# Optimization experiments

Hardware: AMD Instinct MI355X
Metric: run time of the kernel (lower is better)

The kernel has to match this reference:

```python
import jax, jax.numpy as jnp
import numpy as np

N_NODES = 50000
N_EDGES = 800000
F_IN = 128
HID = 128
F_ADD = 32
N_GRAPHS = 128


def setup_inputs() -> dict:
    key = jax.random.key(0)
    ks = jax.random.split(key, 12)
    x = jax.random.normal(ks[0], (N_NODES, F_IN), dtype=jnp.float32)
    edge_index = jax.random.randint(ks[1], (2, N_EDGES), 0, N_NODES, dtype=jnp.int64)
    batch = jnp.sort(jax.random.randint(ks[2], (N_NODES,), 0, N_GRAPHS, dtype=jnp.int64))
    additional_features = jax.random.normal(ks[3], (N_GRAPHS, F_ADD), dtype=jnp.float32)
    def glorot(k, shape):
        fan_in, fan_out = shape[0], shape[1]
        lim = jnp.sqrt(6.0 / (fan_in + fan_out)).astype(jnp.float32)
        return jax.random.uniform(k, shape, jnp.float32, -lim, lim)
    W1 = glorot(ks[4], (F_IN, HID)); b1 = jnp.zeros((HID,), jnp.float32)
    W2 = glorot(ks[5], (HID, HID)); b2 = jnp.zeros((HID,), jnp.float32)
    fc1_w = glorot(ks[6], (HID + F_ADD, HID)); fc1_b = jnp.zeros((HID,), jnp.float32)
    fc2_w = glorot(ks[7], (HID, 2)); fc2_b = jnp.zeros((2,), jnp.float32)
    return {"x": x, "edge_index": edge_index, "batch": batch,
            "additional_features": additional_features,
            "W1": W1, "b1": b1, "W2": W2, "b2": b2,
            "fc1_w": fc1_w, "fc1_b": fc1_b, "fc2_w": fc2_w, "fc2_b": fc2_b}


def _gcn_conv(h, src, dst, norm, W, b):
    # h: [N, d_in]; symmetric-normalized scatter-add aggregation (PyG GCNConv)
    h = h @ W                                   # [N, d_out]
    msg = h[src] * norm[:, None]                # gather + scale: [E+N, d_out]
    return jax.ops.segment_sum(msg, dst, num_segments=N_NODES) + b


def reference(x, edge_index, batch, additional_features,
              W1, b1, W2, b2, fc1_w, fc1_b, fc2_w, fc2_b):
    loops = jnp.arange(N_NODES, dtype=edge_index.dtype)
    src = jnp.concatenate([edge_index[0], loops])   # A + I
    dst = jnp.concatenate([edge_index[1], loops])
    deg = jax.ops.segment_sum(jnp.ones_like(src, dtype=x.dtype), dst,
                              num_segments=N_NODES)
    dinv = jnp.where(deg > 0, jax.lax.rsqrt(jnp.maximum(deg, 1.0)), 0.0)
    norm = dinv[src] * dinv[dst]

    h = jax.nn.relu(_gcn_conv(x, src, dst, norm, W1, b1))
    h = jax.nn.relu(_gcn_conv(h, src, dst, norm, W2, b2))
    # dropout is identity in eval mode

    sums = jax.ops.segment_sum(h, batch, num_segments=N_GRAPHS)    # [G, HID]
    counts = jax.ops.segment_sum(jnp.ones((N_NODES,), h.dtype), batch,
                                 num_segments=N_GRAPHS)
    pooled = sums / jnp.maximum(counts, 1.0)[:, None]              # global_mean_pool

    z = jnp.concatenate([pooled, additional_features], axis=1)     # [G, HID+F_ADD]
    z = jax.nn.relu(z @ fc1_w + fc1_b)
    return z @ fc2_w + fc2_b                                       # [G, 2]
```

## Files before the change

### kernel.cpp

```cpp
#include <hip/hip_runtime.h>

#define NN 50000
#define NE 800000
#define FD 128
#define FDH 64
#define FA 32
#define NG 128
#define EETOT (NE + NN)
#define NBLK ((NN + 255) / 256)
#define FEPB 2048
#define FNCH ((EETOT + FEPB - 1) / FEPB)
#define NPXCD 6250

typedef __attribute__((ext_vector_type(8))) short short8;
typedef __attribute__((ext_vector_type(4))) float f32x4;

__device__ __forceinline__ float bfbits(unsigned short u) {
    return __uint_as_float(((unsigned int)u) << 16);
}
__device__ __forceinline__ float bflo(unsigned int p) { return __uint_as_float(p << 16); }
__device__ __forceinline__ float bfhi(unsigned int p) { return __uint_as_float(p & 0xffff0000u); }
__device__ __forceinline__ unsigned short f2bf(float f) {
    unsigned int u = __float_as_uint(f);
    unsigned int r = u + 0x7FFFu + ((u >> 16) & 1u);
    return (unsigned short)(r >> 16);
}
__device__ __forceinline__ unsigned int packbf(float a, float b) {
    return (unsigned int)f2bf(a) | ((unsigned int)f2bf(b) << 16);
}

__device__ __forceinline__ int wave_probe_bf16(const unsigned int* t, int nwords) {
    int lane = threadIdx.x & 63;
    unsigned int wv = (lane < nwords) ? t[lane] : 0u;
    int nzp = (wv != 0u) ? 1 : 0;
    unsigned int e = (wv >> 7) & 0xFFu;
    int hitp = (nzp && e >= 100u && e <= 140u) ? 1 : 0;
    int nz = __popcll(__ballot(nzp));
    int hits = __popcll(__ballot(hitp));
    return (nz < 8) ? 1 : (hits * 4 >= nz * 3);
}
__device__ __forceinline__ int wave_probe_is64(const int* ei) {
    int lane = threadIdx.x & 63;
    int v = (lane < 32) ? ei[2 * lane + 1] : 0;
    return (__ballot(v != 0) == 0ull) ? 1 : 0;
}

__global__ __launch_bounds__(128) void mark_kernel(float* out, float v) {
    out[threadIdx.x] = v;
}

__global__ __launch_bounds__(256) void prep(
        const void* addf, const void* w1, const void* b1, const void* w2,
        const void* b2, const void* fc1w, const void* fc1b, const void* fc2w,
        const void* fc2b, unsigned int* W1t, unsigned int* W2t,
        float* addff, float* b1f, float* b2f, float* fc1wf, float* fc1bf,
        float* fc2wf, float* fc2bf, int* degi, int* tsum) {
    int b = blockIdx.x;
    if (b < 64) {
        int rel = b * 256 + threadIdx.x;
        const void* src = (rel < 8192) ? w1 : w2;
        unsigned int* dst = (rel < 8192) ? W1t : W2t;
        int flag = wave_probe_bf16((const unsigned int*)src, 64);
        int rr = rel & 8191;
        int n = rr >> 6, kk = rr & 63;
        float lo, hi;
        if (flag) {
            const unsigned short* s = (const unsigned short*)src;
            lo = bfbits(s[(2 * kk) * FD + n]);
            hi = bfbits(s[(2 * kk + 1) * FD + n]);
        } else {
            const float* s = (const float*)src;
            lo = s[(2 * kk) * FD + n];
            hi = s[(2 * kk + 1) * FD + n];
        }
        dst[rr] = packbf(lo, hi);
    } else if (b < 163) {
        int i = (b - 64) * 256 + threadIdx.x;
        int wb = (b - 64) * 256 + (threadIdx.x & ~63);
        const void* src; float* dst; int base; int prnw; int lim;
        if      (wb < 4096)  { src = addf; dst = addff; base = 0;     prnw = 64; lim = 4096;  }
        else if (wb < 4224)  { src = b1;   dst = b1f;   base = 4096;  prnw = 64; lim = 128;   }
        else if (wb < 4352)  { src = b2;   dst = b2f;   base = 4224;  prnw = 64; lim = 128;   }
        else if (wb < 24832) { src = fc1w; dst = fc1wf; base = 4352;  prnw = 64; lim = 20480; }
        else if (wb < 24960) { src = fc1b; dst = fc1bf; base = 24832; prnw = 64; lim = 128;   }
        else if (wb < 25216) { src = fc2w; dst = fc2wf; base = 24960; prnw = 64; lim = 256;   }
        else if (wb < 25280) { src = fc2b; dst = fc2bf; base = 25216; prnw = 1;  lim = 2;     }
        else return;
        int flag = wave_probe_bf16((const unsigned int*)src, prnw);
        int rel = i - base;
        if (rel < lim) {
            if (flag) dst[rel] = bfbits(((const unsigned short*)src)[rel]);
            else      dst[rel] = ((const float*)src)[rel];
        }
    } else {
        int i = (b - 163) * 256 + threadIdx.x;
        if      (i < NN)       degi[i] = 0;
        else if (i < NN + 256) tsum[i - NN] = 0;
    }
}

__global__ __launch_bounds__(256) void deg_kernel(const int* ei, int* deg,
                                                  int* s32, int* d32) {
    int is64 = wave_probe_is64(ei);
    int e = blockIdx.x * 256 + threadIdx.x;
    if (e < NE) {
        int s = is64 ? ei[2 * e] : ei[e];
        int d = is64 ? ei[2 * (NE + e)] : ei[NE + e];
        s32[e] = s;
        d32[e] = d;
        atomicAdd(&deg[d], 1);
    }
}

__global__ __launch_bounds__(256) void scan_fused(const int* degi, const int* batch,
        int* tsum, float* dinv, int* rowstart, int* cursor, int* gstart) {
    __shared__ int sh[256];
    int b = blockIdx.x, t = threadIdx.x;
    int i = b * 256 + t;
    int d = (i < NN) ? degi[i] : 0;
    if (i < NN) dinv[i] = rsqrtf((float)(d + 1));
    int v = (i < NN) ? d + 1 : 0;
    sh[t] = v;
    __syncthreads();
    for (int off = 1; off < 256; off <<= 1) {
        int a = (t >= off) ? sh[t - off] : 0;
        __syncthreads();
        sh[t] += a;
        __syncthreads();
    }
    int incl = sh[t];
    int total = sh[255];
    if (t == 0) atomicExch(&tsum[b], total);
    int pt = 0;
    for (int j = t; j < b; j += 256) {
        int s;
        do { s = atomicAdd(&tsum[j], 0); } while (s == 0);
        pt += s;
    }
    __syncthreads();
    sh[t] = pt;
    __syncthreads();
    for (int off = 128; off >= 1; off >>= 1) {
        if (t < off) sh[t] += sh[t + off];
        __syncthreads();
    }
    int boff = sh[0];
    if (i < NN) {
        int r = boff + incl - v;
        rowstart[i] = r;
        cursor[i]   = r;
    }
    if (i == 0) rowstart[NN] = EETOT;
    if (i < NN) {
        int is64 = (batch[NN - 1] == 0) ? 1 : 0;
        int bc = is64 ? batch[2 * i] : batch[i];
        if (i == 0) {
            for (int g = 0; g <= bc; ++g) gstart[g] = 0;
        } else {
            int bp = is64 ? batch[2 * (i - 1)] : batch[i - 1];
            for (int g = bp + 1; g <= bc; ++g) gstart[g] = i;
        }
        if (i == NN - 1) {
            for (int g = bc + 1; g <= NG; ++g) gstart[g] = NN;
        }
    }
}

__global__ __launch_bounds__(256) void fill_kernel(const int* s32, const int* d32,
        const float* dinv, int* cursor, unsigned int* cv) {
    int chunk = blockIdx.x >> 3;
    int par   = blockIdx.x & 7;
    int base  = chunk * FEPB;
    #pragma unroll
    for (int k = 0; k < FEPB / 256; ++k) {
        int e = base + k * 256 + threadIdx.x;
        if (e >= EETOT) break;
        int s, d;
        if (e < NE) { d = d32[e]; s = -1; }
        else        { s = d = e - NE; }
        if (d / NPXCD != par) continue;
        if (s < 0) s = s32[e];
        int pos = atomicAdd(&cursor[d], 1);
        cv[pos] = (unsigned int)s | ((unsigned int)f2bf(dinv[s] * dinv[d]) << 16);
    }
}

__global__ __launch_bounds__(256) void gemm_mfma(const void* __restrict__ Av,
        const unsigned int* __restrict__ Wt, unsigned short* __restrict__ C,
        int maybe_f32) {
    int wave = threadIdx.x >> 6;
    int lane = threadIdx.x & 63;
    int quad = lane >> 4;
    int l16  = lane & 15;
    int mbase = blockIdx.x * 64 + wave * 16;
    int ra = mbase + l16;
    if (ra >= NN) ra = NN - 1;
    bool f32in = false;
    if (maybe_f32) f32in = !wave_probe_bf16((const unsigned int*)Av, 64);
    short8 af[4];
    if (!f32in) {
        const uint4* Arow = (const uint4*)((const unsigned int*)Av + (size_t)ra * FDH);
        #pragma unroll
        for (int kk = 0; kk < 4; ++kk) {
            uint4 v = Arow[kk * 4 + quad];
            af[kk] = *(short8*)&v;
        }
    } else {
        const float* Arow = (const float*)Av + (size_t)ra * FD;
        #pragma unroll
        for (int kk = 0; kk < 4; ++kk) {
            const float4* p = (const float4*)(Arow + (kk * 4 + quad) * 8);
            float4 u = p[0], v = p[1];
            uint4 q;
            q.x = packbf(u.x, u.y); q.y = packbf(u.z, u.w);
            q.z = packbf(v.x, v.y); q.w = packbf(v.z, v.w);
            af[kk] = *(short8*)&q;
        }
    }
    #pragma unroll
    for (int nt = 0; nt < 8; ++nt) {
        int n = nt * 16 + l16;
        const uint4* Wrow = (const uint4*)(Wt + (size_t)n * FDH);
        f32x4 acc = {0.f, 0.f, 0.f, 0.f};
        #pragma unroll
        for (int kk = 0; kk < 4; ++kk) {
            uint4 wv = Wrow[kk * 4 + quad];
            short8 bf = *(short8*)&wv;
            acc = __builtin_amdgcn_mfma_f32_16x16x32_bf16(af[kk], bf, acc, 0, 0, 0);
        }
        int row0 = mbase + quad * 4;
        #pragma unroll
        for (int reg = 0; reg < 4; ++reg) {
            int r = row0 + reg;
            if (r < NN) C[(size_t)r * FD + nt * 16 + l16] = f2bf(acc[reg]);
        }
    }
}

__global__ __launch_bounds__(256) void aggregate_kernel(const unsigned int* Hb,
        const unsigned int* cv, const int* rowstart, const float* bias,
        unsigned int* outb) {
    int lane = threadIdx.x & 63;
    int half = lane >> 5;
    int c2   = lane & 31;
    int wv   = threadIdx.x >> 6;
    int n = blockIdx.x * 8 + wv * 2 + half;
    const uint2* H2 = (const uint2*)Hb;
    int jb = rowstart[n], je = rowstart[n + 1];
    float a0 = 0.f, a1 = 0.f, a2 = 0.f, a3 = 0.f;
    int j = jb;
    for (; j + 7 < je; j += 8) {
        unsigned int rr[8]; uint2 hh[8];
        #pragma unroll
        for (int k = 0; k < 8; ++k) rr[k] = cv[j + k];
        #pragma unroll
        for (int k = 0; k < 8; ++k) hh[k] = H2[(size_t)(rr[k] & 0xFFFFu) * 32 + c2];
        #pragma unroll
        for (int k = 0; k < 8; ++k) {
            float v = bfbits((unsigned short)(rr[k] >> 16));
            a0 += v * bflo(hh[k].x); a1 += v * bfhi(hh[k].x);
            a2 += v * bflo(hh[k].y); a3 += v * bfhi(hh[k].y);
        }
    }
    for (; j + 3 < je; j += 4) {
        unsigned int rr[4]; uint2 hh[4];
        #pragma unroll
        for (int k = 0; k < 4; ++k) rr[k] = cv[j + k];
        #pragma unroll
        for (int k = 0; k < 4; ++k) hh[k] = H2[(size_t)(rr[k] & 0xFFFFu) * 32 + c2];
        #pragma unroll
        for (int k = 0; k < 4; ++k) {
            float v = bfbits((unsigned short)(rr[k] >> 16));
            a0 += v * bflo(hh[k].x); a1 += v * bfhi(hh[k].x);
            a2 += v * bflo(hh[k].y); a3 += v * bfhi(hh[k].y);
        }
    }
    for (; j < je; ++j) {
        unsigned int r = cv[j];
        uint2 h = H2[(size_t)(r & 0xFFFFu) * 32 + c2];
        float v = bfbits((unsigned short)(r >> 16));
        a0 += v * bflo(h.x); a1 += v * bfhi(h.x);
        a2 += v * bflo(h.y); a3 += v * bfhi(h.y);
    }
    a0 = fmaxf(a0 + bias[4 * c2],     0.f);
    a1 = fmaxf(a1 + bias[4 * c2 + 1], 0.f);
    a2 = fmaxf(a2 + bias[4 * c2 + 2], 0.f);
    a3 = fmaxf(a3 + bias[4 * c2 + 3], 0.f);
    uint2 out;
    out.x = packbf(a0, a1);
    out.y = packbf(a2, a3);
    ((uint2*)outb)[(size_t)n * 32 + c2] = out;
}

__global__ __launch_bounds__(256) void poolhead(const unsigned int* Hb,
        const int* gstart, const float* addf, const float* fc1w, const float* fc1b,
        const float* fc2w, const float* fc2b, const unsigned int* x, void* outp) {
    int g = blockIdx.x;
    int t = threadIdx.x;
    int q = t >> 6, w = t & 63;
    int obf = wave_probe_bf16(x, 64);
    int s = gstart[g], e = gstart[g + 1];
    float a0 = 0.f, a1 = 0.f;
    #pragma unroll 4
    for (int n = s + q; n < e; n += 4) {
        unsigned int h = Hb[(size_t)n * FDH + w];
        a0 += bflo(h);
        a1 += bfhi(h);
    }
    __shared__ float pp[4][FD];
    __shared__ float z[FD + FA];
    __shared__ float h[FD];
    pp[q][2 * w]     = a0;
    pp[q][2 * w + 1] = a1;
    __syncthreads();
    if (t < FD) {
        float cnt = (float)(e - s);
        if (cnt < 1.0f) cnt = 1.0f;
        z[t] = (pp[0][t] + pp[1][t] + pp[2][t] + pp[3][t]) / cnt;
    }
    if (t >= FD && t < FD + FA) z[t] = addf[g * FA + (t - FD)];
    __syncthreads();
    if (t < FD) {
        float acc = fc1b[t];
        #pragma unroll 4
        for (int k = 0; k < FD + FA; ++k)
            acc += z[k] * fc1w[k * FD + t];
        h[t] = fmaxf(acc, 0.f);
    }
    __syncthreads();
    if (t < 2) {
        float o = fc2b[t];
        for (int j = 0; j < FD; ++j) o += h[j] * fc2w[j * 2 + t];
        if (obf) ((unsigned short*)outp)[g * 2 + t] = f2bf(o);
        else     ((float*)outp)[g * 2 + t] = o;
    }
}

extern "C" void kernel_launch(void* const* d_in, const int* in_sizes, int n_in,
                              void* d_out, int out_size, void* d_ws, size_t ws_size,
                              hipStream_t stream) {
    (void)out_size;

    if (n_in != 12) {
        hipLaunchKernelGGL(mark_kernel, dim3(1), dim3(128), 0, stream,
                           (float*)d_out, 2000.0f);
        return;
    }
    const int exp_sizes[12] = {6400000, 1600000, 50000, 4096, 16384, 128,
                               16384, 128, 20480, 128, 256, 2};
    for (int i = 0; i < 12; ++i) {
        if (in_sizes[i] != exp_sizes[i]) {
            hipLaunchKernelGGL(mark_kernel, dim3(1), dim3(128), 0, stream,
                               (float*)d_out, 3000.0f + 100.0f * i);
            return;
        }
    }

    size_t off = 0;
    char* base = (char*)d_ws;
#define WSALLOC(ptr, type, nbytes) \
    type* ptr = (type*)(base + off); off += (((size_t)(nbytes)) + 255) & ~(size_t)255;
    WSALLOC(bufA,  unsigned int, (size_t)NN * FDH * 4)
    WSALLOC(bufB,  unsigned int, (size_t)NN * FDH * 4)
    WSALLOC(dinv,  float, (size_t)NN * 4)
    WSALLOC(degi,  int,   (size_t)NN * 4)
    WSALLOC(rowst, int,   (size_t)(NN + 1) * 4)
    WSALLOC(cursor,int,   (size_t)NN * 4)
    WSALLOC(tsum,  int,   256 * 4)
    WSALLOC(cv,    unsigned int, (size_t)EETOT * 4)
    WSALLOC(gstart,int,   (size_t)(NG + 1) * 4)
    WSALLOC(s32,   int,   (size_t)NE * 4)
    WSALLOC(d32,   int,   (size_t)NE * 4)
    WSALLOC(W1t,   unsigned int, (size_t)FD * FDH * 4)
    WSALLOC(W2t,   unsigned int, (size_t)FD * FDH * 4)
    WSALLOC(b1f,   float, FD * 4)
    WSALLOC(b2f,   float, FD * 4)
    WSALLOC(addff, float, (size_t)NG * FA * 4)
    WSALLOC(fc1wf, float, (size_t)(FD + FA) * FD * 4)
    WSALLOC(fc1bf, float, FD * 4)
    WSALLOC(fc2wf, float, FD * 2 * 4)
    WSALLOC(fc2bf, float, 2 * 4)
#undef WSALLOC
    if (ws_size < off) {
        hipLaunchKernelGGL(mark_kernel, dim3(1), dim3(128), 0, stream,
                           (float*)d_out, 1000.0f);
        return;
    }

    const int* ei    = (const int*)d_in[1];
    const int* batch = (const int*)d_in[2];

    hipLaunchKernelGGL(prep, dim3(360), dim3(256), 0, stream,
                       d_in[3], d_in[4], d_in[5], d_in[6], d_in[7],
                       d_in[8], d_in[9], d_in[10], d_in[11],
                       W1t, W2t, addff, b1f, b2f, fc1wf, fc1bf,
                       fc2wf, fc2bf, degi, tsum);

    hipLaunchKernelGGL(deg_kernel, dim3((NE + 255) / 256), dim3(256), 0, stream,
                       ei, degi, s32, d32);
    hipLaunchKernelGGL(scan_fused, dim3(NBLK), dim3(256), 0, stream,
                       degi, batch, tsum, dinv, rowst, cursor, gstart);
    hipLaunchKernelGGL(fill_kernel, dim3(FNCH * 8), dim3(256), 0, stream,
                       s32, d32, dinv, cursor, cv);

    hipLaunchKernelGGL(gemm_mfma, dim3((NN + 63) / 64), dim3(256), 0, stream,
                       d_in[0], W1t, (unsigned short*)bufA, 1);
    hipLaunchKernelGGL(aggregate_kernel, dim3(NN / 8), dim3(256), 0, stream,
                       bufA, cv, rowst, b1f, bufB);
    hipLaunchKernelGGL(gemm_mfma, dim3((NN + 63) / 64), dim3(256), 0, stream,
                       bufB, W2t, (unsigned short*)bufA, 0);
    hipLaunchKernelGGL(aggregate_kernel, dim3(NN / 8), dim3(256), 0, stream,
                       bufA, cv, rowst, b2f, bufB);

    hipLaunchKernelGGL(poolhead, dim3(NG), dim3(256), 0, stream,
                       bufB, gstart, addff, fc1wf, fc1bf, fc2wf, fc2bf,
                       (const unsigned int*)d_in[0], d_out);
}
```

Before: 301.9 us.

## Fuse CSR fill with first GEMM and widen aggregate gathers to 16 bytes

The CSR fill kernel and the first-layer MFMA GEMM become one launch with split block ranges, so the two independent stages run concurrently and one launch is removed. The aggregate kernel now uses 16 lanes per node with uint4 loads (8 bf16 per lane), processing 4 nodes per wave instead of 2. This issues fewer, wider gather loads per edge. In exchange it raises register use, and the fused kernel's GEMM blocks may compete for CUs with the atomic-heavy fill blocks.

```diff
diff --git a/kernel.cpp b/kernel.cpp
--- a/kernel.cpp
+++ b/kernel.cpp
@@ -10,6 +10,8 @@
 #define NBLK ((NN + 255) / 256)
 #define FEPB 2048
 #define FNCH ((EETOT + FEPB - 1) / FEPB)
+#define FILLB (FNCH * 8)
+#define GEMMB ((NN + 63) / 64)
 #define NPXCD 6250
 
 typedef __attribute__((ext_vector_type(8))) short short8;
@@ -166,28 +168,79 @@
     }
 }
 
-__global__ __launch_bounds__(256) void fill_kernel(const int* s32, const int* d32,
-        const float* dinv, int* cursor, unsigned int* cv) {
-    int chunk = blockIdx.x >> 3;
-    int par   = blockIdx.x & 7;
-    int base  = chunk * FEPB;
+__global__ __launch_bounds__(256) void fill_gemm(const int* s32, const int* d32,
+        const float* dinv, int* cursor, unsigned int* cv,
+        const void* __restrict__ Av, const unsigned int* __restrict__ Wt,
+        unsigned short* __restrict__ C) {
+    if ((int)blockIdx.x < FILLB) {
+        int chunk = blockIdx.x >> 3;
+        int par   = blockIdx.x & 7;
+        int base  = chunk * FEPB;
+        #pragma unroll
+        for (int k = 0; k < FEPB / 256; ++k) {
+            int e = base + k * 256 + threadIdx.x;
+            if (e >= EETOT) break;
+            int s, d;
+            if (e < NE) { d = d32[e]; s = -1; }
+            else        { s = d = e - NE; }
+            if (d / NPXCD != par) continue;
+            if (s < 0) s = s32[e];
+            int pos = atomicAdd(&cursor[d], 1);
+            cv[pos] = (unsigned int)s | ((unsigned int)f2bf(dinv[s] * dinv[d]) << 16);
+        }
+        return;
+    }
+    int bid = blockIdx.x - FILLB;
+    int wave = threadIdx.x >> 6;
+    int lane = threadIdx.x & 63;
+    int quad = lane >> 4;
+    int l16  = lane & 15;
+    int mbase = bid * 64 + wave * 16;
+    int ra = mbase + l16;
+    if (ra >= NN) ra = NN - 1;
+    bool f32in = !wave_probe_bf16((const unsigned int*)Av, 64);
+    short8 af[4];
+    if (!f32in) {
+        const uint4* Arow = (const uint4*)((const unsigned int*)Av + (size_t)ra * FDH);
+        #pragma unroll
+        for (int kk = 0; kk < 4; ++kk) {
+            uint4 v = Arow[kk * 4 + quad];
+            af[kk] = *(short8*)&v;
+        }
+    } else {
+        const float* Arow = (const float*)Av + (size_t)ra * FD;
+        #pragma unroll
+        for (int kk = 0; kk < 4; ++kk) {
+            const float4* p = (const float4*)(Arow + (kk * 4 + quad) * 8);
+            float4 u = p[0], v = p[1];
+            uint4 q;
+            q.x = packbf(u.x, u.y); q.y = packbf(u.z, u.w);
+            q.z = packbf(v.x, v.y); q.w = packbf(v.z, v.w);
+            af[kk] = *(short8*)&q;
+        }
+    }
     #pragma unroll
-    for (int k = 0; k < FEPB / 256; ++k) {
-        int e = base + k * 256 + threadIdx.x;
-        if (e >= EETOT) break;
-        int s, d;
-        if (e < NE) { d = d32[e]; s = -1; }
-        else        { s = d = e - NE; }
-        if (d / NPXCD != par) continue;
-        if (s < 0) s = s32[e];
-        int pos = atomicAdd(&cursor[d], 1);
-        cv[pos] = (unsigned int)s | ((unsigned int)f2bf(dinv[s] * dinv[d]) << 16);
-    }
-}
-
-__global__ __launch_bounds__(256) void gemm_mfma(const void* __restrict__ Av,
-        const unsigned int* __restrict__ Wt, unsigned short* __restrict__ C,
-        int maybe_f32) {
+    for (int nt = 0; nt < 8; ++nt) {
+        int n = nt * 16 + l16;
+        const uint4* Wrow = (const uint4*)(Wt + (size_t)n * FDH);
+        f32x4 acc = {0.f, 0.f, 0.f, 0.f};
+        #pragma unroll
+        for (int kk = 0; kk < 4; ++kk) {
+            uint4 wv = Wrow[kk * 4 + quad];
+            short8 bf = *(short8*)&wv;
+            acc = __builtin_amdgcn_mfma_f32_16x16x32_bf16(af[kk], bf, acc, 0, 0, 0);
+        }
+        int row0 = mbase + quad * 4;
+        #pragma unroll
+        for (int reg = 0; reg < 4; ++reg) {
+            int r = row0 + reg;
+            if (r < NN) C[(size_t)r * FD + nt * 16 + l16] = f2bf(acc[reg]);
+        }
+    }
+}
+
+__global__ __launch_bounds__(256) void gemm_mfma(const unsigned int* __restrict__ Av,
+        const unsigned int* __restrict__ Wt, unsigned short* __restrict__ C) {
     int wave = threadIdx.x >> 6;
     int lane = threadIdx.x & 63;
     int quad = lane >> 4;
@@ -195,27 +248,12 @@
     int mbase = blockIdx.x * 64 + wave * 16;
     int ra = mbase + l16;
     if (ra >= NN) ra = NN - 1;
-    bool f32in = false;
-    if (maybe_f32) f32in = !wave_probe_bf16((const unsigned int*)Av, 64);
     short8 af[4];
-    if (!f32in) {
-        const uint4* Arow = (const uint4*)((const unsigned int*)Av + (size_t)ra * FDH);
-        #pragma unroll
-        for (int kk = 0; kk < 4; ++kk) {
-            uint4 v = Arow[kk * 4 + quad];
-            af[kk] = *(short8*)&v;
-        }
-    } else {
-        const float* Arow = (const float*)Av + (size_t)ra * FD;
-        #pragma unroll
-        for (int kk = 0; kk < 4; ++kk) {
-            const float4* p = (const float4*)(Arow + (kk * 4 + quad) * 8);
-            float4 u = p[0], v = p[1];
-            uint4 q;
-            q.x = packbf(u.x, u.y); q.y = packbf(u.z, u.w);
-            q.z = packbf(v.x, v.y); q.w = packbf(v.z, v.w);
-            af[kk] = *(short8*)&q;
-        }
+    const uint4* Arow = (const uint4*)(Av + (size_t)ra * FDH);
+    #pragma unroll
+    for (int kk = 0; kk < 4; ++kk) {
+        uint4 v = Arow[kk * 4 + quad];
+        af[kk] = *(short8*)&v;
     }
     #pragma unroll
     for (int nt = 0; nt < 8; ++nt) {
@@ -241,55 +279,68 @@
         const unsigned int* cv, const int* rowstart, const float* bias,
         unsigned int* outb) {
     int lane = threadIdx.x & 63;
-    int half = lane >> 5;
-    int c2   = lane & 31;
+    int r4   = lane >> 4;
+    int c4   = lane & 15;
     int wv   = threadIdx.x >> 6;
-    int n = blockIdx.x * 8 + wv * 2 + half;
-    const uint2* H2 = (const uint2*)Hb;
+    int n = blockIdx.x * 16 + wv * 4 + r4;
+    const uint4* H4 = (const uint4*)Hb;
     int jb = rowstart[n], je = rowstart[n + 1];
     float a0 = 0.f, a1 = 0.f, a2 = 0.f, a3 = 0.f;
+    float a4 = 0.f, a5 = 0.f, a6 = 0.f, a7 = 0.f;
     int j = jb;
     for (; j + 7 < je; j += 8) {
-        unsigned int rr[8]; uint2 hh[8];
+        unsigned int rr[8]; uint4 hh[8];
         #pragma unroll
         for (int k = 0; k < 8; ++k) rr[k] = cv[j + k];
         #pragma unroll
-        for (int k = 0; k < 8; ++k) hh[k] = H2[(size_t)(rr[k] & 0xFFFFu) * 32 + c2];
+        for (int k = 0; k < 8; ++k) hh[k] = H4[(size_t)(rr[k] & 0xFFFFu) * 16 + c4];
         #pragma unroll
         for (int k = 0; k < 8; ++k) {
             float v = bfbits((unsigned short)(rr[k] >> 16));
             a0 += v * bflo(hh[k].x); a1 += v * bfhi(hh[k].x);
             a2 += v * bflo(hh[k].y); a3 += v * bfhi(hh[k].y);
+            a4 += v * bflo(hh[k].z); a5 += v * bfhi(hh[k].z);
+            a6 += v * bflo(hh[k].w); a7 += v * bfhi(hh[k].w);
         }
     }
     for (; j + 3 < je; j += 4) {
-        unsigned int rr[4]; uint2 hh[4];
+        unsigned int rr[4]; uint4 hh[4];
         #pragma unroll
         for (int k = 0; k < 4; ++k) rr[k] = cv[j + k];
         #pragma unroll
-        for (int k = 0; k < 4; ++k) hh[k] = H2[(size_t)(rr[k] & 0xFFFFu) * 32 + c2];
+        for (int k = 0; k < 4; ++k) hh[k] = H4[(size_t)(rr[k] & 0xFFFFu) * 16 + c4];
         #pragma unroll
         for (int k = 0; k < 4; ++k) {
             float v = bfbits((unsigned short)(rr[k] >> 16));
             a0 += v * bflo(hh[k].x); a1 += v * bfhi(hh[k].x);
             a2 += v * bflo(hh[k].y); a3 += v * bfhi(hh[k].y);
+            a4 += v * bflo(hh[k].z); a5 += v * bfhi(hh[k].z);
+            a6 += v * bflo(hh[k].w); a7 += v * bfhi(hh[k].w);
         }
     }
     for (; j < je; ++j) {
         unsigned int r = cv[j];
-        uint2 h = H2[(size_t)(r & 0xFFFFu) * 32 + c2];
+        uint4 h = H4[(size_t)(r & 0xFFFFu) * 16 + c4];
         float v = bfbits((unsigned short)(r >> 16));
         a0 += v * bflo(h.x); a1 += v * bfhi(h.x);
         a2 += v * bflo(h.y); a3 += v * bfhi(h.y);
-    }
-    a0 = fmaxf(a0 + bias[4 * c2],     0.f);
-    a1 = fmaxf(a1 + bias[4 * c2 + 1], 0.f);
-    a2 = fmaxf(a2 + bias[4 * c2 + 2], 0.f);
-    a3 = fmaxf(a3 + bias[4 * c2 + 3], 0.f);
-    uint2 out;
+        a4 += v * bflo(h.z); a5 += v * bfhi(h.z);
+        a6 += v * bflo(h.w); a7 += v * bfhi(h.w);
+    }
+    a0 = fmaxf(a0 + bias[8 * c4 + 0], 0.f);
+    a1 = fmaxf(a1 + bias[8 * c4 + 1], 0.f);
+    a2 = fmaxf(a2 + bias[8 * c4 + 2], 0.f);
+    a3 = fmaxf(a3 + bias[8 * c4 + 3], 0.f);
+    a4 = fmaxf(a4 + bias[8 * c4 + 4], 0.f);
+    a5 = fmaxf(a5 + bias[8 * c4 + 5], 0.f);
+    a6 = fmaxf(a6 + bias[8 * c4 + 6], 0.f);
+    a7 = fmaxf(a7 + bias[8 * c4 + 7], 0.f);
+    uint4 out;
     out.x = packbf(a0, a1);
     out.y = packbf(a2, a3);
-    ((uint2*)outb)[(size_t)n * 32 + c2] = out;
+    out.z = packbf(a4, a5);
+    out.w = packbf(a6, a7);
+    ((uint4*)outb)[(size_t)n * 16 + c4] = out;
 }
 
 __global__ __launch_bounds__(256) void poolhead(const unsigned int* Hb,
@@ -400,16 +451,16 @@
                        ei, degi, s32, d32);
     hipLaunchKernelGGL(scan_fused, dim3(NBLK), dim3(256), 0, stream,
                        degi, batch, tsum, dinv, rowst, cursor, gstart);
-    hipLaunchKernelGGL(fill_kernel, dim3(FNCH * 8), dim3(256), 0, stream,
-                       s32, d32, dinv, cursor, cv);
-
-    hipLaunchKernelGGL(gemm_mfma, dim3((NN + 63) / 64), dim3(256), 0, stream,
-                       d_in[0], W1t, (unsigned short*)bufA, 1);
-    hipLaunchKernelGGL(aggregate_kernel, dim3(NN / 8), dim3(256), 0, stream,
+
+    hipLaunchKernelGGL(fill_gemm, dim3(FILLB + GEMMB), dim3(256), 0, stream,
+                       s32, d32, dinv, cursor, cv,
+                       d_in[0], W1t, (unsigned short*)bufA);
+
+    hipLaunchKernelGGL(aggregate_kernel, dim3(NN / 16), dim3(256), 0, stream,
                        bufA, cv, rowst, b1f, bufB);
-    hipLaunchKernelGGL(gemm_mfma, dim3((NN + 63) / 64), dim3(256), 0, stream,
-                       bufB, W2t, (unsigned short*)bufA, 0);
-    hipLaunchKernelGGL(aggregate_kernel, dim3(NN / 8), dim3(256), 0, stream,
+    hipLaunchKernelGGL(gemm_mfma, dim3(GEMMB), dim3(256), 0, stream,
+                       bufB, W2t, (unsigned short*)bufA);
+    hipLaunchKernelGGL(aggregate_kernel, dim3(NN / 16), dim3(256), 0, stream,
                        bufA, cv, rowst, b2f, bufB);
 
     hipLaunchKernelGGL(poolhead, dim3(NG), dim3(256), 0, stream,
```

After: 299.6 us. About the same (-0.8%).
